# Kernel optimization log

Hardware: AMD Instinct MI355X
Metric: run time of the kernel (lower is better)

Reference implementation:

```python
import jax, jax.numpy as jnp
import numpy as np

D_K = 32  # hard-coded in original module


def setup_inputs() -> dict:
    key = jax.random.key(0)
    kq, kk, kv, km = jax.random.split(key, 4)
    B, H, S, D = 4, 12, 2048, D_K
    Q = jax.random.normal(kq, (B, H, S, D), dtype=jnp.float32)
    K = jax.random.normal(kk, (B, H, S, D), dtype=jnp.float32)
    V = jax.random.normal(kv, (B, H, S, D), dtype=jnp.float32)
    attn_mask = jax.random.bernoulli(km, 0.5, (B, H, S, S))
    return {"Q": Q, "K": K, "V": V, "attn_mask": attn_mask}


def tanh_max(a):
    # (exp(a) - exp(-a)) / sum_over_keys(exp(a) + exp(-a))
    ea = jnp.exp(a)
    ena = jnp.exp(-a)
    return (ea - ena) / (ea + ena).sum(axis=-1, keepdims=True)


def reference(Q, K, V, attn_mask):
    # scores: [B,H,S,S]
    scores = jnp.einsum("bhqd,bhkd->bhqk", Q, K) / np.sqrt(D_K).astype(np.float32)
    attn = tanh_max(scores)
    # NOTE: original calls attn.masked_fill(attn_mask, 0.0) WITHOUT assignment
    # (non-in-place), so the mask has no effect. Reproduced faithfully.
    context = jnp.einsum("bhqk,bhkd->bhqd", attn, V)
    return context
```

## Files before the change

kernel.cpp:

```cpp
#include <hip/hip_runtime.h>
#include <hip/hip_bf16.h>
#include <cstdint>
#include <cstddef>


#define SLEN 2048
#define DK   32
#define NBH  48
#define PROW 40

typedef __attribute__((ext_vector_type(8))) short bf16x8;
typedef __attribute__((ext_vector_type(4))) float f32x4;

__device__ __forceinline__ unsigned pk2(float a, float b) {
    __hip_bfloat162 h = __float22bfloat162_rn(make_float2(a, b));
    union { __hip_bfloat162 h2; unsigned u; } cv; cv.h2 = h; return cv.u;
}

__global__ __launch_bounds__(256)
void prep_k(const float* __restrict__ K, unsigned short* __restrict__ Kbf) {
    const int b  = blockIdx.x;
    const int bh = b >> 5, kg = b & 31;
    const int tl = threadIdx.x >> 6, l = threadIdx.x & 63;
    const int t  = kg * 4 + tl;
    const int c  = t >> 1, tb = t & 1;
    const int key = c * 32 + 2 * (l & 15) + tb;
    const float* src = K + ((size_t)bh * SLEN + key) * DK + (l >> 4) * 8;
    float4 a = *(const float4*)src;
    float4 b4 = *(const float4*)(src + 4);
    union { uint4 q; unsigned u[4]; } o;
    o.u[0] = pk2(a.x, a.y);  o.u[1] = pk2(a.z, a.w);
    o.u[2] = pk2(b4.x, b4.y); o.u[3] = pk2(b4.z, b4.w);
    *(uint4*)(Kbf + (((size_t)bh * 128 + t) * 64 + l) * 8) = o.q;
}

__global__ __launch_bounds__(256)
void prep_v(const float* __restrict__ V, unsigned short* __restrict__ VTf) {
    __shared__ float tile[32][33];
    const int b  = blockIdx.x;
    const int bh = b >> 6, c = b & 63;
    const int t  = threadIdx.x;
    {
        const int row = t >> 3, c4 = (t & 7) * 4;
        float4 v4 = *(const float4*)(V + ((size_t)bh * SLEN + c * 32 + row) * DK + c4);
        tile[row][c4 + 0] = v4.x; tile[row][c4 + 1] = v4.y;
        tile[row][c4 + 2] = v4.z; tile[row][c4 + 3] = v4.w;
    }
    __syncthreads();
    const int h = t >> 7, l = (t >> 1) & 63, jh = t & 1;
    const int col = h * 16 + (l & 15);
    const int r0  = (l >> 4) * 8 + jh * 4;
    uint2 u;
    u.x = pk2(tile[r0 + 0][col], tile[r0 + 1][col]);
    u.y = pk2(tile[r0 + 2][col], tile[r0 + 3][col]);
    *(uint2*)(VTf + ((((size_t)bh * 64 + c) * 2 + h) * 64 + l) * 8 + jh * 4) = u;
}

__global__ __launch_bounds__(256, 4)
void attn_mfma(const float* __restrict__ Q, const unsigned short* __restrict__ Kbf,
               const unsigned short* __restrict__ VTf, float* __restrict__ Out) {
    __shared__ __align__(16) unsigned short Pbuf[4][16 * PROW];

    const int tid  = threadIdx.x;
    const int lane = tid & 63;
    const int wv   = tid >> 6;
    const int quad = lane >> 4;
    const int l16  = lane & 15;

    const int b   = blockIdx.x;
    const int xcd = b & 7;
    const int i   = b >> 3;
    const int bh  = xcd * 6 + (i % 6);
    const int qt  = i / 6;
    const int qbase = (qt * 4 + wv) * 16;

    const float sc = 0.17677669529663687f * 1.4426950408889634f;
    const float* qp = Q + ((size_t)bh * SLEN + qbase + l16) * DK + quad * 8;
    float4 qa = *(const float4*)qp;
    float4 qb = *(const float4*)(qp + 4);
    union { bf16x8 v; unsigned u[4]; } aQ;
    aQ.u[0] = pk2(qa.x * sc, qa.y * sc); aQ.u[1] = pk2(qa.z * sc, qa.w * sc);
    aQ.u[2] = pk2(qb.x * sc, qb.y * sc); aQ.u[3] = pk2(qb.z * sc, qb.w * sc);

    const bf16x8* kf = (const bf16x8*)Kbf + (size_t)bh * 128 * 64 + lane;
    const bf16x8* vf = (const bf16x8*)VTf + (size_t)bh * 128 * 64 + lane;

    f32x4 o0 = {0.f, 0.f, 0.f, 0.f};
    f32x4 o1 = {0.f, 0.f, 0.f, 0.f};
    const f32x4 zero = {0.f, 0.f, 0.f, 0.f};
    float den[4] = {0.f, 0.f, 0.f, 0.f};

    unsigned short* pb  = &Pbuf[wv][0];
    unsigned*       pbw = (unsigned*)pb;

    bf16x8 k0 = kf[0], k1 = kf[64];
    bf16x8 v0 = vf[0], v1 = vf[64];

    for (int c = 0; c < 64; ++c) {
        const int cn = (c + 1) & 63;
        bf16x8 nk0 = kf[(size_t)cn * 128];
        bf16x8 nk1 = kf[(size_t)cn * 128 + 64];
        bf16x8 nv0 = vf[(size_t)cn * 128];
        bf16x8 nv1 = vf[(size_t)cn * 128 + 64];

        f32x4 s0 = __builtin_amdgcn_mfma_f32_16x16x32_bf16(aQ.v, k0, zero, 0, 0, 0);
        f32x4 s1 = __builtin_amdgcn_mfma_f32_16x16x32_bf16(aQ.v, k1, zero, 0, 0, 0);

        #pragma unroll
        for (int r = 0; r < 4; ++r) {
            float e0  = __builtin_amdgcn_exp2f(s0[r]);
            float en0 = __builtin_amdgcn_exp2f(-s0[r]);
            float e1  = __builtin_amdgcn_exp2f(s1[r]);
            float en1 = __builtin_amdgcn_exp2f(-s1[r]);
            den[r] += (e0 + en0) + (e1 + en1);
            pbw[(quad * 4 + r) * (PROW / 2) + l16] = pk2(e0 - en0, e1 - en1);
        }

        bf16x8 aP = *(const bf16x8*)(pb + l16 * PROW + quad * 8);

        o0 = __builtin_amdgcn_mfma_f32_16x16x32_bf16(aP, v0, o0, 0, 0, 0);
        o1 = __builtin_amdgcn_mfma_f32_16x16x32_bf16(aP, v1, o1, 0, 0, 0);

        k0 = nk0; k1 = nk1; v0 = nv0; v1 = nv1;
    }

    #pragma unroll
    for (int r = 0; r < 4; ++r) {
        den[r] += __shfl_xor(den[r], 1, 16);
        den[r] += __shfl_xor(den[r], 2, 16);
        den[r] += __shfl_xor(den[r], 4, 16);
        den[r] += __shfl_xor(den[r], 8, 16);
    }

    float* outp = Out + ((size_t)bh * SLEN + qbase) * DK;
    #pragma unroll
    for (int r = 0; r < 4; ++r) {
        float inv = 1.0f / den[r];
        int q = quad * 4 + r;
        outp[(size_t)q * DK + l16]      = o0[r] * inv;
        outp[(size_t)q * DK + 16 + l16] = o1[r] * inv;
    }
}

extern "C" void kernel_launch(void* const* d_in, const int* in_sizes, int n_in,
                              void* d_out, int out_size, void* d_ws, size_t ws_size,
                              hipStream_t stream) {
    const float* Q = (const float*)d_in[0];
    const float* K = (const float*)d_in[1];
    const float* V = (const float*)d_in[2];
    float* Out = (float*)d_out;
    unsigned short* Kbf = (unsigned short*)d_ws;
    unsigned short* VTf = Kbf + (size_t)NBH * SLEN * DK;

    prep_k<<<dim3(NBH * 32), dim3(256), 0, stream>>>(K, Kbf);
    prep_v<<<dim3(NBH * 64), dim3(256), 0, stream>>>(V, VTf);
    attn_mfma<<<dim3(NBH * 32), dim3(256), 0, stream>>>(Q, Kbf, VTf, Out);
}
```

Measured before the change: 934.3 us.

## Split keys across wave pairs, software-pipeline P, and merge K/V prep kernels

The attention kernel now assigns two query tiles per block and splits the key range between wave pairs, then reduces partial outputs and denominators through shared memory. The grid doubles to 3072 blocks for more parallelism. The loop is software-pipelined with a double-buffered P tile, so the exp/pack of one chunk overlaps the PV MFMA of the previous one. The two prep kernels are merged into one launch to cut launch overhead, and launch bounds rise to 6 blocks per CU. The cost is an extra block sync and LDS reduction, plus higher register pressure.

```diff
diff --git a/kernel.cpp b/kernel.cpp
--- a/kernel.cpp
+++ b/kernel.cpp
@@ -8,6 +8,7 @@
 #define DK   32
 #define NBH  48
 #define PROW 40
+#define NCH  32
 
 typedef __attribute__((ext_vector_type(8))) short bf16x8;
 typedef __attribute__((ext_vector_type(4))) float f32x4;
@@ -18,94 +19,86 @@
 }
 
 __global__ __launch_bounds__(256)
-void prep_k(const float* __restrict__ K, unsigned short* __restrict__ Kbf) {
-    const int b  = blockIdx.x;
-    const int bh = b >> 5, kg = b & 31;
-    const int tl = threadIdx.x >> 6, l = threadIdx.x & 63;
-    const int t  = kg * 4 + tl;
-    const int c  = t >> 1, tb = t & 1;
-    const int key = c * 32 + 2 * (l & 15) + tb;
-    const float* src = K + ((size_t)bh * SLEN + key) * DK + (l >> 4) * 8;
-    float4 a = *(const float4*)src;
-    float4 b4 = *(const float4*)(src + 4);
-    union { uint4 q; unsigned u[4]; } o;
-    o.u[0] = pk2(a.x, a.y);  o.u[1] = pk2(a.z, a.w);
-    o.u[2] = pk2(b4.x, b4.y); o.u[3] = pk2(b4.z, b4.w);
-    *(uint4*)(Kbf + (((size_t)bh * 128 + t) * 64 + l) * 8) = o.q;
+void prep_kv(const float* __restrict__ K, const float* __restrict__ V,
+             unsigned short* __restrict__ Kbf, unsigned short* __restrict__ VTf) {
+    if (blockIdx.x < NBH * 32) {
+        const int b  = blockIdx.x;
+        const int bh = b >> 5, kg = b & 31;
+        const int tl = threadIdx.x >> 6, l = threadIdx.x & 63;
+        const int t  = kg * 4 + tl;
+        const int c  = t >> 1, tb = t & 1;
+        const int key = c * 32 + 2 * (l & 15) + tb;
+        const float* src = K + ((size_t)bh * SLEN + key) * DK + (l >> 4) * 8;
+        float4 a = *(const float4*)src;
+        float4 b4 = *(const float4*)(src + 4);
+        union { uint4 q; unsigned u[4]; } o;
+        o.u[0] = pk2(a.x, a.y);  o.u[1] = pk2(a.z, a.w);
+        o.u[2] = pk2(b4.x, b4.y); o.u[3] = pk2(b4.z, b4.w);
+        *(uint4*)(Kbf + (((size_t)bh * 128 + t) * 64 + l) * 8) = o.q;
+    } else {
+        __shared__ float tile[32][33];
+        const int b  = blockIdx.x - NBH * 32;
+        const int bh = b >> 6, c = b & 63;
+        const int t  = threadIdx.x;
+        {
+            const int row = t >> 3, c4 = (t & 7) * 4;
+            float4 v4 = *(const float4*)(V + ((size_t)bh * SLEN + c * 32 + row) * DK + c4);
+            tile[row][c4 + 0] = v4.x; tile[row][c4 + 1] = v4.y;
+            tile[row][c4 + 2] = v4.z; tile[row][c4 + 3] = v4.w;
+        }
+        __syncthreads();
+        const int h = t >> 7, l = (t >> 1) & 63, jh = t & 1;
+        const int col = h * 16 + (l & 15);
+        const int r0  = (l >> 4) * 8 + jh * 4;
+        uint2 u;
+        u.x = pk2(tile[r0 + 0][col], tile[r0 + 1][col]);
+        u.y = pk2(tile[r0 + 2][col], tile[r0 + 3][col]);
+        *(uint2*)(VTf + ((((size_t)bh * 64 + c) * 2 + h) * 64 + l) * 8 + jh * 4) = u;
+    }
 }
 
-__global__ __launch_bounds__(256)
-void prep_v(const float* __restrict__ V, unsigned short* __restrict__ VTf) {
-    __shared__ float tile[32][33];
-    const int b  = blockIdx.x;
-    const int bh = b >> 6, c = b & 63;
-    const int t  = threadIdx.x;
-    {
-        const int row = t >> 3, c4 = (t & 7) * 4;
-        float4 v4 = *(const float4*)(V + ((size_t)bh * SLEN + c * 32 + row) * DK + c4);
-        tile[row][c4 + 0] = v4.x; tile[row][c4 + 1] = v4.y;
-        tile[row][c4 + 2] = v4.z; tile[row][c4 + 3] = v4.w;
-    }
-    __syncthreads();
-    const int h = t >> 7, l = (t >> 1) & 63, jh = t & 1;
-    const int col = h * 16 + (l & 15);
-    const int r0  = (l >> 4) * 8 + jh * 4;
-    uint2 u;
-    u.x = pk2(tile[r0 + 0][col], tile[r0 + 1][col]);
-    u.y = pk2(tile[r0 + 2][col], tile[r0 + 3][col]);
-    *(uint2*)(VTf + ((((size_t)bh * 64 + c) * 2 + h) * 64 + l) * 8 + jh * 4) = u;
-}
-
-__global__ __launch_bounds__(256, 4)
+__global__ __launch_bounds__(256, 6)
 void attn_mfma(const float* __restrict__ Q, const unsigned short* __restrict__ Kbf,
                const unsigned short* __restrict__ VTf, float* __restrict__ Out) {
-    __shared__ __align__(16) unsigned short Pbuf[4][16 * PROW];
+    __shared__ __align__(16) unsigned short Pbuf[4][2][16 * PROW];
+    __shared__ __align__(16) float Red[2][64][12];
 
     const int tid  = threadIdx.x;
     const int lane = tid & 63;
     const int wv   = tid >> 6;
     const int quad = lane >> 4;
     const int l16  = lane & 15;
+    const int qi   = wv >> 1;
+    const int kh   = wv & 1;
 
     const int b   = blockIdx.x;
     const int xcd = b & 7;
     const int i   = b >> 3;
     const int bh  = xcd * 6 + (i % 6);
-    const int qt  = i / 6;
-    const int qbase = (qt * 4 + wv) * 16;
+    const int qp  = i / 6;
+    const int qbase = (qp * 2 + qi) * 16;
 
     const float sc = 0.17677669529663687f * 1.4426950408889634f;
-    const float* qp = Q + ((size_t)bh * SLEN + qbase + l16) * DK + quad * 8;
-    float4 qa = *(const float4*)qp;
-    float4 qb = *(const float4*)(qp + 4);
+    const float* qp_ = Q + ((size_t)bh * SLEN + qbase + l16) * DK + quad * 8;
+    float4 qa = *(const float4*)qp_;
+    float4 qb = *(const float4*)(qp_ + 4);
     union { bf16x8 v; unsigned u[4]; } aQ;
     aQ.u[0] = pk2(qa.x * sc, qa.y * sc); aQ.u[1] = pk2(qa.z * sc, qa.w * sc);
     aQ.u[2] = pk2(qb.x * sc, qb.y * sc); aQ.u[3] = pk2(qb.z * sc, qb.w * sc);
 
-    const bf16x8* kf = (const bf16x8*)Kbf + (size_t)bh * 128 * 64 + lane;
-    const bf16x8* vf = (const bf16x8*)VTf + (size_t)bh * 128 * 64 + lane;
+    const bf16x8* kf = (const bf16x8*)Kbf + (size_t)bh * 8192 + (size_t)kh * 4096 + lane;
+    const bf16x8* vf = (const bf16x8*)VTf + (size_t)bh * 8192 + (size_t)kh * 4096 + lane;
 
     f32x4 o0 = {0.f, 0.f, 0.f, 0.f};
     f32x4 o1 = {0.f, 0.f, 0.f, 0.f};
+    f32x4 den = {0.f, 0.f, 0.f, 0.f};
     const f32x4 zero = {0.f, 0.f, 0.f, 0.f};
-    float den[4] = {0.f, 0.f, 0.f, 0.f};
 
-    unsigned short* pb  = &Pbuf[wv][0];
+    unsigned short* pb  = &Pbuf[wv][0][0];
     unsigned*       pbw = (unsigned*)pb;
 
-    bf16x8 k0 = kf[0], k1 = kf[64];
-    bf16x8 v0 = vf[0], v1 = vf[64];
-
-    for (int c = 0; c < 64; ++c) {
-        const int cn = (c + 1) & 63;
-        bf16x8 nk0 = kf[(size_t)cn * 128];
-        bf16x8 nk1 = kf[(size_t)cn * 128 + 64];
-        bf16x8 nv0 = vf[(size_t)cn * 128];
-        bf16x8 nv1 = vf[(size_t)cn * 128 + 64];
-
-        f32x4 s0 = __builtin_amdgcn_mfma_f32_16x16x32_bf16(aQ.v, k0, zero, 0, 0, 0);
-        f32x4 s1 = __builtin_amdgcn_mfma_f32_16x16x32_bf16(aQ.v, k1, zero, 0, 0, 0);
-
+    auto exppack = [&](const f32x4& s0, const f32x4& s1, int buf) {
+        unsigned* pw = pbw + buf * (16 * PROW / 2);
         #pragma unroll
         for (int r = 0; r < 4; ++r) {
             float e0  = __builtin_amdgcn_exp2f(s0[r]);
@@ -113,15 +106,37 @@
             float e1  = __builtin_amdgcn_exp2f(s1[r]);
             float en1 = __builtin_amdgcn_exp2f(-s1[r]);
             den[r] += (e0 + en0) + (e1 + en1);
-            pbw[(quad * 4 + r) * (PROW / 2) + l16] = pk2(e0 - en0, e1 - en1);
+            pw[(quad * 4 + r) * (PROW / 2) + l16] = pk2(e0 - en0, e1 - en1);
         }
+    };
+    auto readP = [&](int buf) -> bf16x8 {
+        return *(const bf16x8*)(pb + buf * (16 * PROW) + l16 * PROW + quad * 8);
+    };
 
-        bf16x8 aP = *(const bf16x8*)(pb + l16 * PROW + quad * 8);
+    bf16x8 ka = kf[0], kb = kf[64];
+    bf16x8 v_cur0 = vf[0], v_cur1 = vf[64];
+    f32x4 s0 = __builtin_amdgcn_mfma_f32_16x16x32_bf16(aQ.v, ka, zero, 0, 0, 0);
+    f32x4 s1 = __builtin_amdgcn_mfma_f32_16x16x32_bf16(aQ.v, kb, zero, 0, 0, 0);
+    ka = kf[128]; kb = kf[192];
+    exppack(s0, s1, 0);
 
-        o0 = __builtin_amdgcn_mfma_f32_16x16x32_bf16(aP, v0, o0, 0, 0, 0);
-        o1 = __builtin_amdgcn_mfma_f32_16x16x32_bf16(aP, v1, o1, 0, 0, 0);
-
-        k0 = nk0; k1 = nk1; v0 = nv0; v1 = nv1;
+    for (int c = 0; c < NCH - 1; ++c) {
+        s0 = __builtin_amdgcn_mfma_f32_16x16x32_bf16(aQ.v, ka, zero, 0, 0, 0);
+        s1 = __builtin_amdgcn_mfma_f32_16x16x32_bf16(aQ.v, kb, zero, 0, 0, 0);
+        const int c2 = (c + 2) & (NCH - 1);
+        ka = kf[(size_t)c2 * 128]; kb = kf[(size_t)c2 * 128 + 64];
+        bf16x8 v_nxt0 = vf[(size_t)(c + 1) * 128];
+        bf16x8 v_nxt1 = vf[(size_t)(c + 1) * 128 + 64];
+        bf16x8 aP = readP(c & 1);
+        exppack(s0, s1, (c + 1) & 1);
+        o0 = __builtin_amdgcn_mfma_f32_16x16x32_bf16(aP, v_cur0, o0, 0, 0, 0);
+        o1 = __builtin_amdgcn_mfma_f32_16x16x32_bf16(aP, v_cur1, o1, 0, 0, 0);
+        v_cur0 = v_nxt0; v_cur1 = v_nxt1;
+    }
+    {
+        bf16x8 aP = readP((NCH - 1) & 1);
+        o0 = __builtin_amdgcn_mfma_f32_16x16x32_bf16(aP, v_cur0, o0, 0, 0, 0);
+        o1 = __builtin_amdgcn_mfma_f32_16x16x32_bf16(aP, v_cur1, o1, 0, 0, 0);
     }
 
     #pragma unroll
@@ -132,13 +147,28 @@
         den[r] += __shfl_xor(den[r], 8, 16);
     }
 
-    float* outp = Out + ((size_t)bh * SLEN + qbase) * DK;
-    #pragma unroll
-    for (int r = 0; r < 4; ++r) {
-        float inv = 1.0f / den[r];
-        int q = quad * 4 + r;
-        outp[(size_t)q * DK + l16]      = o0[r] * inv;
-        outp[(size_t)q * DK + 16 + l16] = o1[r] * inv;
+    if (kh == 1) {
+        float* r = &Red[qi][lane][0];
+        *(f32x4*)(r + 0) = o0;
+        *(f32x4*)(r + 4) = o1;
+        *(f32x4*)(r + 8) = den;
+    }
+    __syncthreads();
+    if (kh == 0) {
+        const float* r = &Red[qi][lane][0];
+        f32x4 p0 = *(const f32x4*)(r + 0);
+        f32x4 p1 = *(const f32x4*)(r + 4);
+        f32x4 pd = *(const f32x4*)(r + 8);
+        o0 += p0; o1 += p1; den += pd;
+
+        float* outp = Out + ((size_t)bh * SLEN + qbase) * DK;
+        #pragma unroll
+        for (int rr = 0; rr < 4; ++rr) {
+            float inv = 1.0f / den[rr];
+            int q = quad * 4 + rr;
+            outp[(size_t)q * DK + l16]      = o0[rr] * inv;
+            outp[(size_t)q * DK + 16 + l16] = o1[rr] * inv;
+        }
     }
 }
 
@@ -152,7 +182,6 @@
     unsigned short* Kbf = (unsigned short*)d_ws;
     unsigned short* VTf = Kbf + (size_t)NBH * SLEN * DK;
 
-    prep_k<<<dim3(NBH * 32), dim3(256), 0, stream>>>(K, Kbf);
-    prep_v<<<dim3(NBH * 64), dim3(256), 0, stream>>>(V, VTf);
-    attn_mfma<<<dim3(NBH * 32), dim3(256), 0, stream>>>(Q, Kbf, VTf, Out);
+    prep_kv<<<dim3(NBH * 32 + NBH * 64), dim3(256), 0, stream>>>(K, V, Kbf, VTf);
+    attn_mfma<<<dim3(3072), dim3(256), 0, stream>>>(Q, Kbf, VTf, Out);
 }
```

Result: no change. 926.4 us (-0.8%).

## Split keys across wave pairs with 32-query tiles and merge prep kernels

Applied to the files above, without the earlier changes.

Each wave now handles 32 query rows (two Q fragments) over half of the key range, so every K/V fragment load feeds twice as many MFMAs. The two key-halves are combined through a shared-memory reduction of the partial outputs and denominators, followed by a block barrier. The K and V prep kernels are merged into one launch. This trades more registers and LDS per wave, plus a barrier and reduction step, for less global/L2 traffic per unit of compute and one fewer launch.

```diff
diff --git a/kernel.cpp b/kernel.cpp
--- a/kernel.cpp
+++ b/kernel.cpp
@@ -8,6 +8,7 @@
 #define DK   32
 #define NBH  48
 #define PROW 40
+#define NCH  32
 
 typedef __attribute__((ext_vector_type(8))) short bf16x8;
 typedef __attribute__((ext_vector_type(4))) float f32x4;
@@ -18,127 +19,170 @@
 }
 
 __global__ __launch_bounds__(256)
-void prep_k(const float* __restrict__ K, unsigned short* __restrict__ Kbf) {
-    const int b  = blockIdx.x;
-    const int bh = b >> 5, kg = b & 31;
-    const int tl = threadIdx.x >> 6, l = threadIdx.x & 63;
-    const int t  = kg * 4 + tl;
-    const int c  = t >> 1, tb = t & 1;
-    const int key = c * 32 + 2 * (l & 15) + tb;
-    const float* src = K + ((size_t)bh * SLEN + key) * DK + (l >> 4) * 8;
-    float4 a = *(const float4*)src;
-    float4 b4 = *(const float4*)(src + 4);
-    union { uint4 q; unsigned u[4]; } o;
-    o.u[0] = pk2(a.x, a.y);  o.u[1] = pk2(a.z, a.w);
-    o.u[2] = pk2(b4.x, b4.y); o.u[3] = pk2(b4.z, b4.w);
-    *(uint4*)(Kbf + (((size_t)bh * 128 + t) * 64 + l) * 8) = o.q;
-}
-
-__global__ __launch_bounds__(256)
-void prep_v(const float* __restrict__ V, unsigned short* __restrict__ VTf) {
-    __shared__ float tile[32][33];
-    const int b  = blockIdx.x;
-    const int bh = b >> 6, c = b & 63;
-    const int t  = threadIdx.x;
-    {
-        const int row = t >> 3, c4 = (t & 7) * 4;
-        float4 v4 = *(const float4*)(V + ((size_t)bh * SLEN + c * 32 + row) * DK + c4);
-        tile[row][c4 + 0] = v4.x; tile[row][c4 + 1] = v4.y;
-        tile[row][c4 + 2] = v4.z; tile[row][c4 + 3] = v4.w;
-    }
-    __syncthreads();
-    const int h = t >> 7, l = (t >> 1) & 63, jh = t & 1;
-    const int col = h * 16 + (l & 15);
-    const int r0  = (l >> 4) * 8 + jh * 4;
-    uint2 u;
-    u.x = pk2(tile[r0 + 0][col], tile[r0 + 1][col]);
-    u.y = pk2(tile[r0 + 2][col], tile[r0 + 3][col]);
-    *(uint2*)(VTf + ((((size_t)bh * 64 + c) * 2 + h) * 64 + l) * 8 + jh * 4) = u;
+void prep_kv(const float* __restrict__ K, const float* __restrict__ V,
+             unsigned short* __restrict__ Kbf, unsigned short* __restrict__ VTf) {
+    if (blockIdx.x < NBH * 32) {
+        const int b  = blockIdx.x;
+        const int bh = b >> 5, kg = b & 31;
+        const int tl = threadIdx.x >> 6, l = threadIdx.x & 63;
+        const int t  = kg * 4 + tl;
+        const int c  = t >> 1, tb = t & 1;
+        const int key = c * 32 + 2 * (l & 15) + tb;
+        const float* src = K + ((size_t)bh * SLEN + key) * DK + (l >> 4) * 8;
+        float4 a = *(const float4*)src;
+        float4 b4 = *(const float4*)(src + 4);
+        union { uint4 q; unsigned u[4]; } o;
+        o.u[0] = pk2(a.x, a.y);  o.u[1] = pk2(a.z, a.w);
+        o.u[2] = pk2(b4.x, b4.y); o.u[3] = pk2(b4.z, b4.w);
+        *(uint4*)(Kbf + (((size_t)bh * 128 + t) * 64 + l) * 8) = o.q;
+    } else {
+        __shared__ float tile[32][33];
+        const int b  = blockIdx.x - NBH * 32;
+        const int bh = b >> 6, c = b & 63;
+        const int t  = threadIdx.x;
+        {
+            const int row = t >> 3, c4 = (t & 7) * 4;
+            float4 v4 = *(const float4*)(V + ((size_t)bh * SLEN + c * 32 + row) * DK + c4);
+            tile[row][c4 + 0] = v4.x; tile[row][c4 + 1] = v4.y;
+            tile[row][c4 + 2] = v4.z; tile[row][c4 + 3] = v4.w;
+        }
+        __syncthreads();
+        const int h = t >> 7, l = (t >> 1) & 63, jh = t & 1;
+        const int col = h * 16 + (l & 15);
+        const int r0  = (l >> 4) * 8 + jh * 4;
+        uint2 u;
+        u.x = pk2(tile[r0 + 0][col], tile[r0 + 1][col]);
+        u.y = pk2(tile[r0 + 2][col], tile[r0 + 3][col]);
+        *(uint2*)(VTf + ((((size_t)bh * 64 + c) * 2 + h) * 64 + l) * 8 + jh * 4) = u;
+    }
 }
 
 __global__ __launch_bounds__(256, 4)
 void attn_mfma(const float* __restrict__ Q, const unsigned short* __restrict__ Kbf,
                const unsigned short* __restrict__ VTf, float* __restrict__ Out) {
-    __shared__ __align__(16) unsigned short Pbuf[4][16 * PROW];
+    __shared__ __align__(16) unsigned short Pbuf[4][32 * PROW];
+    __shared__ __align__(16) float Red[2][64][24];
 
     const int tid  = threadIdx.x;
     const int lane = tid & 63;
     const int wv   = tid >> 6;
     const int quad = lane >> 4;
     const int l16  = lane & 15;
+    const int qi   = wv >> 1;
+    const int kh   = wv & 1;
 
     const int b   = blockIdx.x;
     const int xcd = b & 7;
     const int i   = b >> 3;
     const int bh  = xcd * 6 + (i % 6);
-    const int qt  = i / 6;
-    const int qbase = (qt * 4 + wv) * 16;
+    const int j   = i / 6;
+    const int qbase = (j * 2 + qi) * 32;
 
     const float sc = 0.17677669529663687f * 1.4426950408889634f;
-    const float* qp = Q + ((size_t)bh * SLEN + qbase + l16) * DK + quad * 8;
-    float4 qa = *(const float4*)qp;
-    float4 qb = *(const float4*)(qp + 4);
-    union { bf16x8 v; unsigned u[4]; } aQ;
-    aQ.u[0] = pk2(qa.x * sc, qa.y * sc); aQ.u[1] = pk2(qa.z * sc, qa.w * sc);
-    aQ.u[2] = pk2(qb.x * sc, qb.y * sc); aQ.u[3] = pk2(qb.z * sc, qb.w * sc);
-
-    const bf16x8* kf = (const bf16x8*)Kbf + (size_t)bh * 128 * 64 + lane;
-    const bf16x8* vf = (const bf16x8*)VTf + (size_t)bh * 128 * 64 + lane;
-
-    f32x4 o0 = {0.f, 0.f, 0.f, 0.f};
-    f32x4 o1 = {0.f, 0.f, 0.f, 0.f};
-    const f32x4 zero = {0.f, 0.f, 0.f, 0.f};
-    float den[4] = {0.f, 0.f, 0.f, 0.f};
+    union { bf16x8 v; unsigned u[4]; } aQ0, aQ1;
+    {
+        const float* qp0 = Q + ((size_t)bh * SLEN + qbase + l16) * DK + quad * 8;
+        float4 qa = *(const float4*)qp0;
+        float4 qb = *(const float4*)(qp0 + 4);
+        aQ0.u[0] = pk2(qa.x * sc, qa.y * sc); aQ0.u[1] = pk2(qa.z * sc, qa.w * sc);
+        aQ0.u[2] = pk2(qb.x * sc, qb.y * sc); aQ0.u[3] = pk2(qb.z * sc, qb.w * sc);
+        const float* qp1 = qp0 + 16 * DK;
+        float4 qc = *(const float4*)qp1;
+        float4 qd = *(const float4*)(qp1 + 4);
+        aQ1.u[0] = pk2(qc.x * sc, qc.y * sc); aQ1.u[1] = pk2(qc.z * sc, qc.w * sc);
+        aQ1.u[2] = pk2(qd.x * sc, qd.y * sc); aQ1.u[3] = pk2(qd.z * sc, qd.w * sc);
+    }
+
+    const bf16x8* kf = (const bf16x8*)Kbf + ((size_t)bh * 128 + kh * 64) * 64 + lane;
+    const bf16x8* vf = (const bf16x8*)VTf + ((size_t)bh * 128 + kh * 64) * 64 + lane;
+
+    f32x4 o00 = {0,0,0,0}, o01 = {0,0,0,0};
+    f32x4 o10 = {0,0,0,0}, o11 = {0,0,0,0};
+    f32x4 den0 = {0,0,0,0}, den1 = {0,0,0,0};
+    const f32x4 zero = {0,0,0,0};
 
     unsigned short* pb  = &Pbuf[wv][0];
     unsigned*       pbw = (unsigned*)pb;
 
     bf16x8 k0 = kf[0], k1 = kf[64];
-    bf16x8 v0 = vf[0], v1 = vf[64];
-
-    for (int c = 0; c < 64; ++c) {
-        const int cn = (c + 1) & 63;
-        bf16x8 nk0 = kf[(size_t)cn * 128];
-        bf16x8 nk1 = kf[(size_t)cn * 128 + 64];
-        bf16x8 nv0 = vf[(size_t)cn * 128];
-        bf16x8 nv1 = vf[(size_t)cn * 128 + 64];
-
-        f32x4 s0 = __builtin_amdgcn_mfma_f32_16x16x32_bf16(aQ.v, k0, zero, 0, 0, 0);
-        f32x4 s1 = __builtin_amdgcn_mfma_f32_16x16x32_bf16(aQ.v, k1, zero, 0, 0, 0);
+
+    for (int c = 0; c < NCH; ++c) {
+        f32x4 s00 = __builtin_amdgcn_mfma_f32_16x16x32_bf16(aQ0.v, k0, zero, 0, 0, 0);
+        f32x4 s01 = __builtin_amdgcn_mfma_f32_16x16x32_bf16(aQ0.v, k1, zero, 0, 0, 0);
+        f32x4 s10 = __builtin_amdgcn_mfma_f32_16x16x32_bf16(aQ1.v, k0, zero, 0, 0, 0);
+        f32x4 s11 = __builtin_amdgcn_mfma_f32_16x16x32_bf16(aQ1.v, k1, zero, 0, 0, 0);
+
+        bf16x8 v0 = vf[(size_t)c * 128];
+        bf16x8 v1 = vf[(size_t)c * 128 + 64];
+        const int cn = (c + 1) & (NCH - 1);
+        k0 = kf[(size_t)cn * 128];
+        k1 = kf[(size_t)cn * 128 + 64];
 
         #pragma unroll
         for (int r = 0; r < 4; ++r) {
-            float e0  = __builtin_amdgcn_exp2f(s0[r]);
-            float en0 = __builtin_amdgcn_exp2f(-s0[r]);
-            float e1  = __builtin_amdgcn_exp2f(s1[r]);
-            float en1 = __builtin_amdgcn_exp2f(-s1[r]);
-            den[r] += (e0 + en0) + (e1 + en1);
+            float e0  = __builtin_amdgcn_exp2f(s00[r]);
+            float en0 = __builtin_amdgcn_exp2f(-s00[r]);
+            float e1  = __builtin_amdgcn_exp2f(s01[r]);
+            float en1 = __builtin_amdgcn_exp2f(-s01[r]);
+            den0[r] += (e0 + en0) + (e1 + en1);
             pbw[(quad * 4 + r) * (PROW / 2) + l16] = pk2(e0 - en0, e1 - en1);
         }
-
-        bf16x8 aP = *(const bf16x8*)(pb + l16 * PROW + quad * 8);
-
-        o0 = __builtin_amdgcn_mfma_f32_16x16x32_bf16(aP, v0, o0, 0, 0, 0);
-        o1 = __builtin_amdgcn_mfma_f32_16x16x32_bf16(aP, v1, o1, 0, 0, 0);
-
-        k0 = nk0; k1 = nk1; v0 = nv0; v1 = nv1;
+        #pragma unroll
+        for (int r = 0; r < 4; ++r) {
+            float e0  = __builtin_amdgcn_exp2f(s10[r]);
+            float en0 = __builtin_amdgcn_exp2f(-s10[r]);
+            float e1  = __builtin_amdgcn_exp2f(s11[r]);
+            float en1 = __builtin_amdgcn_exp2f(-s11[r]);
+            den1[r] += (e0 + en0) + (e1 + en1);
+            pbw[(16 + quad * 4 + r) * (PROW / 2) + l16] = pk2(e0 - en0, e1 - en1);
+        }
+
+        bf16x8 aP0 = *(const bf16x8*)(pb + l16 * PROW + quad * 8);
+        bf16x8 aP1 = *(const bf16x8*)(pb + (16 + l16) * PROW + quad * 8);
+
+        o00 = __builtin_amdgcn_mfma_f32_16x16x32_bf16(aP0, v0, o00, 0, 0, 0);
+        o01 = __builtin_amdgcn_mfma_f32_16x16x32_bf16(aP0, v1, o01, 0, 0, 0);
+        o10 = __builtin_amdgcn_mfma_f32_16x16x32_bf16(aP1, v0, o10, 0, 0, 0);
+        o11 = __builtin_amdgcn_mfma_f32_16x16x32_bf16(aP1, v1, o11, 0, 0, 0);
     }
 
     #pragma unroll
     for (int r = 0; r < 4; ++r) {
-        den[r] += __shfl_xor(den[r], 1, 16);
-        den[r] += __shfl_xor(den[r], 2, 16);
-        den[r] += __shfl_xor(den[r], 4, 16);
-        den[r] += __shfl_xor(den[r], 8, 16);
-    }
-
-    float* outp = Out + ((size_t)bh * SLEN + qbase) * DK;
-    #pragma unroll
-    for (int r = 0; r < 4; ++r) {
-        float inv = 1.0f / den[r];
-        int q = quad * 4 + r;
-        outp[(size_t)q * DK + l16]      = o0[r] * inv;
-        outp[(size_t)q * DK + 16 + l16] = o1[r] * inv;
+        den0[r] += __shfl_xor(den0[r], 1, 16);
+        den0[r] += __shfl_xor(den0[r], 2, 16);
+        den0[r] += __shfl_xor(den0[r], 4, 16);
+        den0[r] += __shfl_xor(den0[r], 8, 16);
+        den1[r] += __shfl_xor(den1[r], 1, 16);
+        den1[r] += __shfl_xor(den1[r], 2, 16);
+        den1[r] += __shfl_xor(den1[r], 4, 16);
+        den1[r] += __shfl_xor(den1[r], 8, 16);
+    }
+
+    if (kh == 1) {
+        float* r = &Red[qi][lane][0];
+        *(f32x4*)(r +  0) = o00; *(f32x4*)(r +  4) = o01;
+        *(f32x4*)(r +  8) = o10; *(f32x4*)(r + 12) = o11;
+        *(f32x4*)(r + 16) = den0; *(f32x4*)(r + 20) = den1;
+    }
+    __syncthreads();
+    if (kh == 0) {
+        const float* r = &Red[qi][lane][0];
+        o00 += *(const f32x4*)(r +  0); o01 += *(const f32x4*)(r +  4);
+        o10 += *(const f32x4*)(r +  8); o11 += *(const f32x4*)(r + 12);
+        den0 += *(const f32x4*)(r + 16); den1 += *(const f32x4*)(r + 20);
+
+        float* outp = Out + ((size_t)bh * SLEN + qbase) * DK;
+        #pragma unroll
+        for (int rr = 0; rr < 4; ++rr) {
+            float inv0 = 1.0f / den0[rr];
+            float inv1 = 1.0f / den1[rr];
+            int q0 = quad * 4 + rr;
+            int q1 = 16 + quad * 4 + rr;
+            outp[(size_t)q0 * DK + l16]      = o00[rr] * inv0;
+            outp[(size_t)q0 * DK + 16 + l16] = o01[rr] * inv0;
+            outp[(size_t)q1 * DK + l16]      = o10[rr] * inv1;
+            outp[(size_t)q1 * DK + 16 + l16] = o11[rr] * inv1;
+        }
     }
 }
 
@@ -152,7 +196,6 @@
     unsigned short* Kbf = (unsigned short*)d_ws;
     unsigned short* VTf = Kbf + (size_t)NBH * SLEN * DK;
 
-    prep_k<<<dim3(NBH * 32), dim3(256), 0, stream>>>(K, Kbf);
-    prep_v<<<dim3(NBH * 64), dim3(256), 0, stream>>>(V, VTf);
-    attn_mfma<<<dim3(NBH * 32), dim3(256), 0, stream>>>(Q, Kbf, VTf, Out);
-}
+    prep_kv<<<dim3(NBH * 32 + NBH * 64), dim3(256), 0, stream>>>(K, V, Kbf, VTf);
+    attn_mfma<<<dim3(1536), dim3(256), 0, stream>>>(Q, Kbf, VTf, Out);
+}
```

New measurement: 926.9 us. No clear change (-0.8%).
